# Kernel optimization log

Hardware: AMD Instinct MI355X
Metric: run time of the kernel (lower is better)

The kernel has to match this reference:

```python
import jax, jax.numpy as jnp
import numpy as np

B, N, DIN, DOUT, H = 32, 1024, 512, 512, 8
DH = DOUT // H  # attn_dim = 64


def setup_inputs() -> dict:
    key = jax.random.key(0)
    k1, k2, k3, k4, k5 = jax.random.split(key, 5)
    X = jax.random.normal(k1, (B, N, DIN), dtype=jnp.float32)
    # adjacency mask (sparse-ish 0/1 pattern, self-loops included)
    A = (jax.random.uniform(k2, (B, N, N)) < 0.05).astype(jnp.float32)
    A = jnp.maximum(A, jnp.eye(N, dtype=jnp.float32)[None])
    # per-head projection weights/biases and bilinear coefficient matrices
    # (xavier_normal init as in param_initializer)
    std_w = np.sqrt(2.0 / (DIN + DH))
    std_c = np.sqrt(2.0 / (DH + DH))
    Wp = jax.random.normal(k3, (H, DIN, DH), dtype=jnp.float32) * std_w
    bp = jnp.zeros((H, DH), dtype=jnp.float32)
    C = jax.random.normal(k4, (H, DH, DH), dtype=jnp.float32) * std_c
    return {"X": X, "A": A, "Wp": Wp, "bp": bp, "C": C}


def reference(X, A, Wp, bp, C):
    # per-head linear projection: [B,H,N,DH]
    Xp = jnp.einsum('bnd,hdk->bhnk', X, Wp) + bp[None, :, None, :]
    # bilinear transform: torch.einsum('akj,ij->aki') == Xp @ C.T per head
    Xc = jnp.einsum('bhnk,hjk->bhnj', Xp, C)
    # attention scores [B,H,N,N], masked by adjacency, tanh
    # (dropout is identity in eval mode)
    attn = jnp.tanh(A[:, None] * jnp.einsum('bhnj,bhmj->bhnm', Xc, Xp))
    # aggregate: [B,H,N,DH]
    Xh = jnp.einsum('bhnm,bhmk->bhnk', attn, Xp)
    # concat heads along feature dim (head order matches torch.cat), then relu
    out = jnp.moveaxis(Xh, 1, 2).reshape(X.shape[0], X.shape[1], -1)
    return jax.nn.relu(out)
```

## Files before the change

### kernel.cpp

```cpp
#include <hip/hip_runtime.h>
#include <hip/hip_bf16.h>

typedef __attribute__((ext_vector_type(8))) _Float16 half8;
typedef __attribute__((ext_vector_type(4))) _Float16 half4;
typedef __attribute__((ext_vector_type(4))) float f32x4;

#define B_ 32
#define N_ 1024
#define DIN_ 512
#define H_ 8
#define DH_ 64

__device__ __forceinline__ float tanh_e(float x) {
    float e = __builtin_amdgcn_exp2f(x * 2.885390081777927f);
    float r = __builtin_amdgcn_rcpf(e + 1.f);
    return fmaf(-2.f, r, 1.f);
}

__global__ __launch_bounds__(256) void pack_mask(const float* __restrict__ A,
                                                 unsigned long long* __restrict__ Abits) {
    int tid = blockIdx.x * 256 + threadIdx.x;
    int wave = tid >> 6;
    int lane = threadIdx.x & 63;
    float a = A[(size_t)wave * 64 + lane];
    unsigned long long m = __ballot(a != 0.f);
    if (lane == 0) Abits[wave] = m;
}

__global__ __launch_bounds__(256) void prep_w(const float* __restrict__ Wp,
                                              const float* __restrict__ C,
                                              _Float16* __restrict__ WT,
                                              _Float16* __restrict__ Cb) {
    int gid = blockIdx.x * 256 + threadIdx.x;
    if (gid < H_ * DH_ * DIN_) {
        int h = gid >> 15;
        int n = (gid >> 9) & 63;
        int k = gid & 511;
        WT[gid] = (_Float16)Wp[((size_t)(h * DIN_ + k)) * DH_ + n];
    } else {
        int cid = gid - H_ * DH_ * DIN_;
        if (cid < H_ * DH_ * DH_) Cb[cid] = (_Float16)C[cid];
    }
}

__global__ __launch_bounds__(256) void proj_gemm(const float* __restrict__ X,
                                                 const float* __restrict__ bp,
                                                 const _Float16* __restrict__ WT,
                                                 _Float16* __restrict__ Xp) {
    __shared__ _Float16 Xb[64][72];

    int tid = threadIdx.x;
    int lane = tid & 63, w = tid >> 6;
    int blk = blockIdx.x;
    int b = blk >> 5;
    int n0 = ((blk >> 1) & 15) * 64;
    int h = (blk & 1) * 4 + w;

    int r = tid >> 2, q = tid & 3;
    const float* xrow = X + ((size_t)b * N_ + n0 + r) * DIN_ + q * 16;

    f32x4 acc[4][4] = {};

    for (int kc = 0; kc < 8; ++kc) {
        float4 v0 = *(const float4*)(xrow + kc * 64 + 0);
        float4 v1 = *(const float4*)(xrow + kc * 64 + 4);
        float4 v2 = *(const float4*)(xrow + kc * 64 + 8);
        float4 v3 = *(const float4*)(xrow + kc * 64 + 12);
        half8 h0 = {(_Float16)v0.x, (_Float16)v0.y, (_Float16)v0.z, (_Float16)v0.w,
                    (_Float16)v1.x, (_Float16)v1.y, (_Float16)v1.z, (_Float16)v1.w};
        half8 h1 = {(_Float16)v2.x, (_Float16)v2.y, (_Float16)v2.z, (_Float16)v2.w,
                    (_Float16)v3.x, (_Float16)v3.y, (_Float16)v3.z, (_Float16)v3.w};
        *(half8*)&Xb[r][q * 16] = h0;
        *(half8*)&Xb[r][q * 16 + 8] = h1;
        __syncthreads();

#pragma unroll
        for (int ks = 0; ks < 2; ++ks) {
            half8 a[4];
#pragma unroll
            for (int m = 0; m < 4; ++m)
                a[m] = *(const half8*)&Xb[m * 16 + (lane & 15)][ks * 32 + (lane >> 4) * 8];
#pragma unroll
            for (int f = 0; f < 4; ++f) {
                half8 bb = *(const half8*)(WT + ((size_t)(h * 64 + f * 16 + (lane & 15))) * DIN_
                                           + kc * 64 + ks * 32 + (lane >> 4) * 8);
#pragma unroll
                for (int m = 0; m < 4; ++m)
                    acc[m][f] = __builtin_amdgcn_mfma_f32_16x16x32_f16(a[m], bb, acc[m][f], 0, 0, 0);
            }
        }
        __syncthreads();
    }

    size_t bh = (size_t)(b * 8 + h);
#pragma unroll
    for (int f = 0; f < 4; ++f) {
        int col = f * 16 + (lane & 15);
        float bias = bp[h * 64 + col];
#pragma unroll
        for (int m = 0; m < 4; ++m) {
            int row = m * 16 + ((lane >> 4) << 2);
#pragma unroll
            for (int j = 0; j < 4; ++j) {
                Xp[(bh * N_ + n0 + row + j) * DH_ + col] = (_Float16)(acc[m][f][j] + bias);
            }
        }
    }
}

__global__ __launch_bounds__(256) void bil_kernel(const _Float16* __restrict__ Xp,
                                                  const _Float16* __restrict__ Cb,
                                                  _Float16* __restrict__ Xc,
                                                  _Float16* __restrict__ XpT) {
    __shared__ _Float16 Xs[64][72];

    int tid = threadIdx.x;
    int lane = tid & 63, w = tid >> 6;
    int blk = blockIdx.x;
    int bh = blk >> 4;
    int n0 = (blk & 15) * 64;
    int h = bh & 7;

    int r = tid >> 2, q = tid & 3;
    const half8* src = (const half8*)(Xp + ((size_t)bh * N_ + n0 + r) * DH_ + q * 16);
    *(half8*)&Xs[r][q * 16] = src[0];
    *(half8*)&Xs[r][q * 16 + 8] = src[1];
    __syncthreads();

    f32x4 acc[4] = {{0,0,0,0},{0,0,0,0},{0,0,0,0},{0,0,0,0}};
#pragma unroll
    for (int ks = 0; ks < 2; ++ks) {
        half8 a = *(const half8*)&Xs[w * 16 + (lane & 15)][ks * 32 + (lane >> 4) * 8];
#pragma unroll
        for (int f = 0; f < 4; ++f) {
            half8 bb = *(const half8*)(Cb + ((size_t)(h * DH_ + f * 16 + (lane & 15))) * DH_
                                       + ks * 32 + (lane >> 4) * 8);
            acc[f] = __builtin_amdgcn_mfma_f32_16x16x32_f16(a, bb, acc[f], 0, 0, 0);
        }
    }
    int rb = w * 16 + ((lane >> 4) << 2);
#pragma unroll
    for (int f = 0; f < 4; ++f) {
        int col = f * 16 + (lane & 15);
#pragma unroll
        for (int j = 0; j < 4; ++j)
            Xc[((size_t)bh * N_ + n0 + rb + j) * DH_ + col] = (_Float16)acc[f][j];
    }

    {
        int d = (lane & 3) * 16 + (lane >> 2);
        __align__(16) _Float16 tmp[16];
#pragma unroll
        for (int i = 0; i < 16; ++i) tmp[i] = Xs[w * 16 + i][d];
        _Float16* dst = XpT + ((size_t)bh * DH_ + d) * N_ + n0 + w * 16;
        *(half8*)dst = *(half8*)tmp;
        *(half8*)(dst + 8) = *(half8*)(tmp + 8);
    }
}

__global__ __launch_bounds__(256) void attn_kernel(const _Float16* __restrict__ Xp,
                                                   const _Float16* __restrict__ Xc,
                                                   const _Float16* __restrict__ XpT,
                                                   const unsigned long long* __restrict__ Abits,
                                                   float* __restrict__ out) {
    __shared__ _Float16 Kb[64][72];
    __shared__ _Float16 Vt[64][72];
    __shared__ _Float16 Ps[64][76];

    int tid = threadIdx.x;
    int lane = tid & 63, w = tid >> 6;
    int blk = blockIdx.x;
    int bh = blk >> 4;
    int q0 = (blk & 15) * 64;
    int b = bh >> 3, h = bh & 7;

    const _Float16* qbase = Xc + ((size_t)bh * N_ + q0 + w * 16 + (lane & 15)) * DH_ + (lane >> 4) * 8;
    half8 qa0 = *(const half8*)qbase;
    half8 qa1 = *(const half8*)(qbase + 32);

    f32x4 oacc[4] = {{0,0,0,0},{0,0,0,0},{0,0,0,0},{0,0,0,0}};
    int r = tid >> 2, q = tid & 3;
    int rb = w * 16 + ((lane >> 4) << 2);
    int c16 = lane & 15;

    for (int mt = 0; mt < 16; ++mt) {
        __syncthreads();
        const half8* ksrc = (const half8*)(Xp + ((size_t)bh * N_ + mt * 64 + r) * DH_ + q * 16);
        half8 k0 = ksrc[0], k1 = ksrc[1];
        const half8* vsrc = (const half8*)(XpT + ((size_t)bh * DH_ + r) * N_ + mt * 64 + q * 16);
        half8 v0 = vsrc[0], v1 = vsrc[1];
        *(half8*)&Kb[r][q * 16] = k0;
        *(half8*)&Kb[r][q * 16 + 8] = k1;
        *(half8*)&Vt[r][q * 16] = v0;
        *(half8*)&Vt[r][q * 16 + 8] = v1;
        __syncthreads();

        f32x4 s[4] = {{0,0,0,0},{0,0,0,0},{0,0,0,0},{0,0,0,0}};
#pragma unroll
        for (int f = 0; f < 4; ++f) {
            half8 kb0 = *(const half8*)&Kb[f * 16 + c16][(lane >> 4) * 8];
            s[f] = __builtin_amdgcn_mfma_f32_16x16x32_f16(qa0, kb0, s[f], 0, 0, 0);
            half8 kb1 = *(const half8*)&Kb[f * 16 + c16][32 + (lane >> 4) * 8];
            s[f] = __builtin_amdgcn_mfma_f32_16x16x32_f16(qa1, kb1, s[f], 0, 0, 0);
        }

#pragma unroll
        for (int j = 0; j < 4; ++j) {
            unsigned long long m0 = Abits[((size_t)b * N_ + q0 + rb + j) * 16 + mt] >> c16;
            unsigned lo = (unsigned)m0, hi = (unsigned)(m0 >> 32);
            unsigned bit0 = lo & 1u, bit1 = (lo >> 16) & 1u;
            unsigned bit2 = hi & 1u, bit3 = (hi >> 16) & 1u;
            float t0 = tanh_e(s[0][j]);
            float t1 = tanh_e(s[1][j]);
            float t2 = tanh_e(s[2][j]);
            float t3 = tanh_e(s[3][j]);
            Ps[rb + j][c16]      = (_Float16)(bit0 ? t0 : 0.f);
            Ps[rb + j][16 + c16] = (_Float16)(bit1 ? t1 : 0.f);
            Ps[rb + j][32 + c16] = (_Float16)(bit2 ? t2 : 0.f);
            Ps[rb + j][48 + c16] = (_Float16)(bit3 ? t3 : 0.f);
        }
        __syncthreads();

#pragma unroll
        for (int ks = 0; ks < 2; ++ks) {
            half8 pa = *(const half8*)&Ps[w * 16 + c16][ks * 32 + (lane >> 4) * 8];
#pragma unroll
            for (int f = 0; f < 4; ++f) {
                half8 vb = *(const half8*)&Vt[f * 16 + c16][ks * 32 + (lane >> 4) * 8];
                oacc[f] = __builtin_amdgcn_mfma_f32_16x16x32_f16(pa, vb, oacc[f], 0, 0, 0);
            }
        }
    }

#pragma unroll
    for (int f = 0; f < 4; ++f) {
        int col = h * DH_ + f * 16 + c16;
#pragma unroll
        for (int j = 0; j < 4; ++j) {
            out[((size_t)b * N_ + q0 + rb + j) * 512 + col] = fmaxf(oacc[f][j], 0.f);
        }
    }
}

extern "C" void kernel_launch(void* const* d_in, const int* in_sizes, int n_in,
                              void* d_out, int out_size, void* d_ws, size_t ws_size,
                              hipStream_t stream) {
    const float* X  = (const float*)d_in[0];
    const float* A  = (const float*)d_in[1];
    const float* Wp = (const float*)d_in[2];
    const float* bp = (const float*)d_in[3];
    const float* C  = (const float*)d_in[4];
    float* out = (float*)d_out;

    char* ws = (char*)d_ws;
    unsigned long long* Abits = (unsigned long long*)ws;
    _Float16* WT  = (_Float16*)(ws + 4u * 1024 * 1024);
    _Float16* Cb  = (_Float16*)(ws + 4u * 1024 * 1024 + 512 * 1024);
    _Float16* Xp  = (_Float16*)(ws + 5u * 1024 * 1024);
    _Float16* Xc  = (_Float16*)(ws + 37u * 1024 * 1024);
    _Float16* XpT = (_Float16*)(ws + 69u * 1024 * 1024);

    pack_mask<<<(B_ * N_ * N_) / (64 * 4), 256, 0, stream>>>(A, Abits);
    prep_w<<<(H_ * DH_ * DIN_ + H_ * DH_ * DH_ + 255) / 256, 256, 0, stream>>>(Wp, C, WT, Cb);
    proj_gemm<<<B_ * 16 * 2, 256, 0, stream>>>(X, bp, WT, Xp);
    bil_kernel<<<B_ * H_ * 16, 256, 0, stream>>>(Xp, Cb, Xc, XpT);
    attn_kernel<<<B_ * H_ * 16, 256, 0, stream>>>(Xp, Xc, XpT, Abits, out);
}
```

Measured before the change: 493.0 us.

## Keep attention probabilities in registers and read K/V directly from global

Removes all shared-memory staging and the three __syncthreads per key tile in the attention kernel. The score MFMA now has its operands swapped, producing S transposed, so its accumulator layout already matches the A-operand layout of a 16x16x16 MFMA. Tanh-masked probabilities are packed to fp16 in registers and fed straight into the PV MFMAs, with K and V fragments loaded per wave from global memory. The cost is redundant global/L2 traffic, since each of the four waves loads the same K/V tiles, and narrower 8-byte V loads.

```diff
diff --git a/kernel.cpp b/kernel.cpp
--- a/kernel.cpp
+++ b/kernel.cpp
@@ -3,6 +3,7 @@
 
 typedef __attribute__((ext_vector_type(8))) _Float16 half8;
 typedef __attribute__((ext_vector_type(4))) _Float16 half4;
+typedef __attribute__((ext_vector_type(2))) unsigned uint2v;
 typedef __attribute__((ext_vector_type(4))) float f32x4;
 
 #define B_ 32
@@ -15,6 +16,13 @@
     float e = __builtin_amdgcn_exp2f(x * 2.885390081777927f);
     float r = __builtin_amdgcn_rcpf(e + 1.f);
     return fmaf(-2.f, r, 1.f);
+}
+
+__device__ __forceinline__ half4 pack4(float a, float b, float c, float d) {
+    auto lo = __builtin_amdgcn_cvt_pkrtz(a, b);
+    auto hi = __builtin_amdgcn_cvt_pkrtz(c, d);
+    uint2v u = { __builtin_bit_cast(unsigned, lo), __builtin_bit_cast(unsigned, hi) };
+    return __builtin_bit_cast(half4, u);
 }
 
 __global__ __launch_bounds__(256) void pack_mask(const float* __restrict__ A,
@@ -163,81 +171,80 @@
                                                    const _Float16* __restrict__ XpT,
                                                    const unsigned long long* __restrict__ Abits,
                                                    float* __restrict__ out) {
-    __shared__ _Float16 Kb[64][72];
-    __shared__ _Float16 Vt[64][72];
-    __shared__ _Float16 Ps[64][76];
-
     int tid = threadIdx.x;
     int lane = tid & 63, w = tid >> 6;
+    int hi = lane >> 4;
+    int c16 = lane & 15;
     int blk = blockIdx.x;
     int bh = blk >> 4;
     int q0 = (blk & 15) * 64;
     int b = bh >> 3, h = bh & 7;
 
-    const _Float16* qbase = Xc + ((size_t)bh * N_ + q0 + w * 16 + (lane & 15)) * DH_ + (lane >> 4) * 8;
+    const _Float16* qbase = Xc + ((size_t)bh * N_ + q0 + w * 16 + c16) * DH_ + hi * 8;
     half8 qa0 = *(const half8*)qbase;
     half8 qa1 = *(const half8*)(qbase + 32);
 
+    const _Float16* kbase = Xp + ((size_t)bh * N_ + c16) * DH_ + hi * 8;
+    const _Float16* vb0 = XpT + ((size_t)bh * DH_ + 0  + c16) * N_ + hi * 4;
+    const _Float16* vb1 = XpT + ((size_t)bh * DH_ + 16 + c16) * N_ + hi * 4;
+    const _Float16* vb2 = XpT + ((size_t)bh * DH_ + 32 + c16) * N_ + hi * 4;
+    const _Float16* vb3 = XpT + ((size_t)bh * DH_ + 48 + c16) * N_ + hi * 4;
+    const unsigned long long* mbase = Abits + ((size_t)b * N_ + q0 + w * 16 + c16) * 16;
+
     f32x4 oacc[4] = {{0,0,0,0},{0,0,0,0},{0,0,0,0},{0,0,0,0}};
-    int r = tid >> 2, q = tid & 3;
-    int rb = w * 16 + ((lane >> 4) << 2);
-    int c16 = lane & 15;
 
     for (int mt = 0; mt < 16; ++mt) {
-        __syncthreads();
-        const half8* ksrc = (const half8*)(Xp + ((size_t)bh * N_ + mt * 64 + r) * DH_ + q * 16);
-        half8 k0 = ksrc[0], k1 = ksrc[1];
-        const half8* vsrc = (const half8*)(XpT + ((size_t)bh * DH_ + r) * N_ + mt * 64 + q * 16);
-        half8 v0 = vsrc[0], v1 = vsrc[1];
-        *(half8*)&Kb[r][q * 16] = k0;
-        *(half8*)&Kb[r][q * 16 + 8] = k1;
-        *(half8*)&Vt[r][q * 16] = v0;
-        *(half8*)&Vt[r][q * 16 + 8] = v1;
-        __syncthreads();
-
+        const _Float16* kmt = kbase + mt * 4096;
         f32x4 s[4] = {{0,0,0,0},{0,0,0,0},{0,0,0,0},{0,0,0,0}};
 #pragma unroll
         for (int f = 0; f < 4; ++f) {
-            half8 kb0 = *(const half8*)&Kb[f * 16 + c16][(lane >> 4) * 8];
-            s[f] = __builtin_amdgcn_mfma_f32_16x16x32_f16(qa0, kb0, s[f], 0, 0, 0);
-            half8 kb1 = *(const half8*)&Kb[f * 16 + c16][32 + (lane >> 4) * 8];
-            s[f] = __builtin_amdgcn_mfma_f32_16x16x32_f16(qa1, kb1, s[f], 0, 0, 0);
-        }
-
+            half8 k0 = *(const half8*)(kmt + f * 1024);
+            half8 k1 = *(const half8*)(kmt + f * 1024 + 32);
+            s[f] = __builtin_amdgcn_mfma_f32_16x16x32_f16(k0, qa0, s[f], 0, 0, 0);
+            s[f] = __builtin_amdgcn_mfma_f32_16x16x32_f16(k1, qa1, s[f], 0, 0, 0);
+        }
+
+        half4 vf0[4], vf1[4], vf2[4], vf3[4];
+#pragma unroll
+        for (int f = 0; f < 4; ++f) {
+            vf0[f] = *(const half4*)(vb0 + mt * 64 + f * 16);
+            vf1[f] = *(const half4*)(vb1 + mt * 64 + f * 16);
+            vf2[f] = *(const half4*)(vb2 + mt * 64 + f * 16);
+            vf3[f] = *(const half4*)(vb3 + mt * 64 + f * 16);
+        }
+
+        unsigned long long m64 = mbase[mt] >> (hi * 4);
+        unsigned mlo = (unsigned)m64;
+        unsigned mhi32 = (unsigned)(m64 >> 32);
+
+        half4 pa[4];
+#pragma unroll
+        for (int f = 0; f < 4; ++f) {
+            unsigned dw = (f & 2) ? mhi32 : mlo;
+            int bb = (f & 1) * 16;
+            float t0 = tanh_e(s[f][0]) * (float)((dw >> bb) & 1u);
+            float t1 = tanh_e(s[f][1]) * (float)((dw >> (bb + 1)) & 1u);
+            float t2 = tanh_e(s[f][2]) * (float)((dw >> (bb + 2)) & 1u);
+            float t3 = tanh_e(s[f][3]) * (float)((dw >> (bb + 3)) & 1u);
+            pa[f] = pack4(t0, t1, t2, t3);
+        }
+
+#pragma unroll
+        for (int f = 0; f < 4; ++f) {
+            oacc[0] = __builtin_amdgcn_mfma_f32_16x16x16f16(pa[f], vf0[f], oacc[0], 0, 0, 0);
+            oacc[1] = __builtin_amdgcn_mfma_f32_16x16x16f16(pa[f], vf1[f], oacc[1], 0, 0, 0);
+            oacc[2] = __builtin_amdgcn_mfma_f32_16x16x16f16(pa[f], vf2[f], oacc[2], 0, 0, 0);
+            oacc[3] = __builtin_amdgcn_mfma_f32_16x16x16f16(pa[f], vf3[f], oacc[3], 0, 0, 0);
+        }
+    }
+
+    int rb = w * 16 + hi * 4;
+#pragma unroll
+    for (int fo = 0; fo < 4; ++fo) {
+        int col = h * DH_ + fo * 16 + c16;
 #pragma unroll
         for (int j = 0; j < 4; ++j) {
-            unsigned long long m0 = Abits[((size_t)b * N_ + q0 + rb + j) * 16 + mt] >> c16;
-            unsigned lo = (unsigned)m0, hi = (unsigned)(m0 >> 32);
-            unsigned bit0 = lo & 1u, bit1 = (lo >> 16) & 1u;
-            unsigned bit2 = hi & 1u, bit3 = (hi >> 16) & 1u;
-            float t0 = tanh_e(s[0][j]);
-            float t1 = tanh_e(s[1][j]);
-            float t2 = tanh_e(s[2][j]);
-            float t3 = tanh_e(s[3][j]);
-            Ps[rb + j][c16]      = (_Float16)(bit0 ? t0 : 0.f);
-            Ps[rb + j][16 + c16] = (_Float16)(bit1 ? t1 : 0.f);
-            Ps[rb + j][32 + c16] = (_Float16)(bit2 ? t2 : 0.f);
-            Ps[rb + j][48 + c16] = (_Float16)(bit3 ? t3 : 0.f);
-        }
-        __syncthreads();
-
-#pragma unroll
-        for (int ks = 0; ks < 2; ++ks) {
-            half8 pa = *(const half8*)&Ps[w * 16 + c16][ks * 32 + (lane >> 4) * 8];
-#pragma unroll
-            for (int f = 0; f < 4; ++f) {
-                half8 vb = *(const half8*)&Vt[f * 16 + c16][ks * 32 + (lane >> 4) * 8];
-                oacc[f] = __builtin_amdgcn_mfma_f32_16x16x32_f16(pa, vb, oacc[f], 0, 0, 0);
-            }
-        }
-    }
-
-#pragma unroll
-    for (int f = 0; f < 4; ++f) {
-        int col = h * DH_ + f * 16 + c16;
-#pragma unroll
-        for (int j = 0; j < 4; ++j) {
-            out[((size_t)b * N_ + q0 + rb + j) * 512 + col] = fmaxf(oacc[f][j], 0.f);
+            out[((size_t)b * N_ + q0 + rb + j) * 512 + col] = fmaxf(oacc[fo][j], 0.f);
         }
     }
 }
```

After: 1.042 ms. +111.3%, slower.
